# Performance work log

Measured on AMD Instinct MI355X. Metric: run time of the kernel, lower is better.

The kernel has to match this reference:

```python
import jax, jax.numpy as jnp
import numpy as np

NUM_HEADS = 16


def setup_inputs() -> dict:
    key = jax.random.key(0)
    ks = jax.random.split(key, 6)
    B, S, E = 2, 2048, 1024
    scale = 1.0 / np.sqrt(E)
    return {
        "x": jax.random.normal(ks[0], (B, S, E), dtype=jnp.float32),
        "mask": jnp.ones((B, S), dtype=jnp.int32),
        "Wq": jax.random.normal(ks[1], (E, E), dtype=jnp.float32) * scale,
        "bq": jnp.zeros((E,), dtype=jnp.float32),
        "Wk": jax.random.normal(ks[2], (E, E), dtype=jnp.float32) * scale,
        "bk": jnp.zeros((E,), dtype=jnp.float32),
        "Wv": jax.random.normal(ks[3], (E, E), dtype=jnp.float32) * scale,
        "bv": jnp.zeros((E,), dtype=jnp.float32),
        "Wo": jax.random.normal(ks[4], (E, E), dtype=jnp.float32) * scale,
        "bo": jnp.zeros((E,), dtype=jnp.float32),
    }


def reference(x, mask, Wq, bq, Wk, bk, Wv, bv, Wo, bo):
    B, S, E = x.shape
    H = NUM_HEADS
    D = E // H

    def heads(t):  # [B,S,E] -> [B,H,S,D]
        return t.reshape(B, S, H, D).transpose(0, 2, 1, 3)

    q = heads(x @ Wq + bq)
    k = heads(x @ Wk + bk)
    v = heads(x @ Wv + bv)

    # scaled dot-product scores [B,H,S,S]
    scores = jnp.einsum("bhsd,bhtd->bhst", q, k) / jnp.sqrt(jnp.float32(D))
    m = mask.astype(jnp.float32)[:, None, None, :]  # key-side padding mask
    scores = scores + (-1e9) * (1.0 - m)
    weights = jax.nn.softmax(scores, axis=-1)
    attn = jnp.einsum("bhst,bhtd->bhsd", weights, v)

    concat = attn.transpose(0, 2, 1, 3).reshape(B, S, E)
    return concat @ Wo + bo
```

## Files before the change

kernel.cpp:

```cpp
#include <hip/hip_runtime.h>
#include <stdint.h>

#define E_DIM   1024
#define HNUM    16
#define DH      64
#define BATCH   2
#define SEQ     2048
#define M_TOT   (BATCH*SEQ)
#define LOG2E   1.44269504088896340736f

typedef __bf16 bf16x8 __attribute__((ext_vector_type(8)));
typedef __bf16 bf16x4 __attribute__((ext_vector_type(4)));
typedef float  f32x4  __attribute__((ext_vector_type(4)));
typedef float  f32x16 __attribute__((ext_vector_type(16)));
typedef unsigned short u16;
typedef unsigned int   u32;
typedef unsigned long long u64;
typedef u16 u16x8 __attribute__((ext_vector_type(8)));
typedef u32 u32x2 __attribute__((ext_vector_type(2)));
typedef u32 u32x4 __attribute__((ext_vector_type(4)));

__device__ __forceinline__ u16 f2bf(float f) {
    u32 u = __builtin_bit_cast(u32, f);
    u32 r = 0x7FFFu + ((u >> 16) & 1u);
    return (u16)((u + r) >> 16);
}

__device__ __forceinline__ void gload_lds16(const u16* g, u16* l) {
    __builtin_amdgcn_global_load_lds(
        (const __attribute__((address_space(1))) u32*)g,
        (__attribute__((address_space(3))) u32*)l, 16, 0, 0);
}

__device__ __forceinline__ u32 cvt_pk_bf16(float lo, float hi) {
    u32 r;
    asm("v_cvt_pk_bf16_f32 %0, %1, %2" : "=v"(r) : "v"(lo), "v"(hi));
    return r;
}

#define MFMA16(a,b,c) __builtin_amdgcn_mfma_f32_16x16x32_bf16((a),(b),(c),0,0,0)
#define MFMA32(a,b,c) __builtin_amdgcn_mfma_f32_32x32x16_bf16((a),(b),(c),0,0,0)

__global__ __launch_bounds__(256) void cast_x_kernel(const float* __restrict__ x,
                                                     u16* __restrict__ out, int n) {
    int idx = (blockIdx.x * 256 + threadIdx.x) * 4;
    if (idx < n) {
        float4 v = *reinterpret_cast<const float4*>(x + idx);
        ushort4 o;
        o.x = f2bf(v.x); o.y = f2bf(v.y); o.z = f2bf(v.z); o.w = f2bf(v.w);
        *reinterpret_cast<ushort4*>(out + idx) = o;
    }
}

__global__ __launch_bounds__(256) void maskbits_kernel(const int* __restrict__ mask,
                                                       u64* __restrict__ bits) {
    int i = blockIdx.x * 256 + threadIdx.x;
    u64 bl = __ballot(mask[i] != 0);
    if ((i & 63) == 0) bits[i >> 6] = bl;
}

__global__ void wtrans_kernel(const float* __restrict__ w0, const float* __restrict__ w1,
                              const float* __restrict__ w2, const float* __restrict__ w3,
                              u16* __restrict__ out) {
    __shared__ float tile[32][33];
    const float* w = blockIdx.z == 0 ? w0 : blockIdx.z == 1 ? w1 : blockIdx.z == 2 ? w2 : w3;
    const int n0 = blockIdx.x * 32, k0 = blockIdx.y * 32;
    #pragma unroll
    for (int j = 0; j < 4; j++) {
        int k = k0 + threadIdx.y + j * 8;
        tile[threadIdx.y + j * 8][threadIdx.x] = w[(size_t)k * E_DIM + n0 + threadIdx.x];
    }
    __syncthreads();
    u16* o = out + (size_t)blockIdx.z * E_DIM * E_DIM;
    #pragma unroll
    for (int j = 0; j < 4; j++) {
        int n = n0 + threadIdx.y + j * 8;
        o[(size_t)n * E_DIM + k0 + threadIdx.x] = f2bf(tile[threadIdx.x][threadIdx.y + j * 8]);
    }
}

template <typename OutT>
__global__ __launch_bounds__(256) void gemm_kernel(
    const u16* __restrict__ A, const u16* __restrict__ Bt_base, OutT* __restrict__ C_base,
    const float* __restrict__ bias0, const float* __restrict__ bias1,
    const float* __restrict__ bias2, float scale0, int Mdim) {
    const int z = blockIdx.z;
    const u16* Bt = Bt_base + (size_t)z * E_DIM * E_DIM;
    OutT* C = C_base + (size_t)z * Mdim * E_DIM;
    const float* bias = (z == 0) ? bias0 : (z == 1 ? bias1 : bias2);
    const float scale = (z == 0) ? scale0 : 1.0f;

    __shared__ __align__(16) u16 Als[128 * 32];
    __shared__ __align__(16) u16 Bls[128 * 32];

    const int tid = threadIdx.x;
    const int lane = tid & 63;
    const int w = tid >> 6;
    const int wr = (w >> 1) * 64, wc = (w & 1) * 64;
    const int tm = blockIdx.y * 128, tn = blockIdx.x * 128;
    const int r4 = tid >> 2;
    const int c8 = (tid & 3) * 8;

    f32x4 acc[4][4] = {};

    for (int k0 = 0; k0 < E_DIM; k0 += 32) {
        gload_lds16(A + (size_t)(tm + r4) * E_DIM + k0 + c8, Als + tid * 8);
        gload_lds16(A + (size_t)(tm + 64 + r4) * E_DIM + k0 + c8, Als + 2048 + tid * 8);
        gload_lds16(Bt + (size_t)(tn + r4) * E_DIM + k0 + c8, Bls + tid * 8);
        gload_lds16(Bt + (size_t)(tn + 64 + r4) * E_DIM + k0 + c8, Bls + 2048 + tid * 8);
        __syncthreads();
        const int lr = lane & 15, lg = lane >> 4;
        bf16x8 af[4], bfr[4];
        #pragma unroll
        for (int m = 0; m < 4; m++)
            af[m] = *reinterpret_cast<const bf16x8*>(Als + (wr + m * 16 + lr) * 32 + lg * 8);
        #pragma unroll
        for (int n = 0; n < 4; n++)
            bfr[n] = *reinterpret_cast<const bf16x8*>(Bls + (wc + n * 16 + lr) * 32 + lg * 8);
        #pragma unroll
        for (int m = 0; m < 4; m++)
            #pragma unroll
            for (int n = 0; n < 4; n++)
                acc[m][n] = MFMA16(af[m], bfr[n], acc[m][n]);
        __syncthreads();
    }

    const int lr = lane & 15, lg = lane >> 4;
    #pragma unroll
    for (int m = 0; m < 4; m++) {
        #pragma unroll
        for (int n = 0; n < 4; n++) {
            const int col = tn + wc + n * 16 + lr;
            const float bv = bias[col];
            #pragma unroll
            for (int r = 0; r < 4; r++) {
                const int row = tm + wr + m * 16 + lg * 4 + r;
                float v = (acc[m][n][r] + bv) * scale;
                if constexpr (sizeof(OutT) == 2) {
                    C[(size_t)row * E_DIM + col] = f2bf(v);
                } else {
                    C[(size_t)row * E_DIM + col] = v;
                }
            }
        }
    }
}

__global__ __launch_bounds__(512) void attn_kernel(
    const u16* __restrict__ Q, const u16* __restrict__ K, const u16* __restrict__ V,
    const u64* __restrict__ mbits, u16* __restrict__ PO, float* __restrict__ lws) {
    __shared__ __align__(16) u16 Kls[4][64 * 64];
    __shared__ __align__(16) u16 Vt[2][64 * 64];

    const int tid = threadIdx.x;
    const int lane = tid & 63;
    const int wave = tid >> 6;
    const int sub = wave >> 2;
    const int wg = wave & 3;
    const int hi = lane >> 5;
    const int l31 = lane & 31;
    const int n = blockIdx.x;
    const int g = n & 63, qt = n >> 6;
    const int h = g & 15, zz = g >> 4;
    const int b = zz >> 1, half = zz & 1;

    const int qrow = b * SEQ + qt * 256 + sub * 128 + wg * 32 + l31;
    bf16x8 qf[4];
    #pragma unroll
    for (int kc = 0; kc < 4; kc++)
        qf[kc] = *reinterpret_cast<const bf16x8*>(Q + (size_t)qrow * E_DIM + h * DH + kc * 16 + hi * 8);

    const int krow = (l31 & 3) | ((l31 & 4) << 1) | ((l31 & 8) >> 1) | (l31 & 16);
    const u32 ksw = (u32)(krow & 7) << 4;
    u32 koff[4];
    #pragma unroll
    for (int kc = 0; kc < 4; kc++)
        koff[kc] = (((u32)krow * 128) + (u32)kc * 32 + (u32)hi * 16) ^ ksw;

    const int krA = tid >> 3;
    const int kcA = (tid & 7) ^ (krA & 7);
    const size_t kgoff = (size_t)krA * E_DIM + kcA * 8;

    const int t8 = tid & 255;
    const int vhalf = tid >> 8;
    const int vc = t8 & 7;
    const int vsg = ((t8 >> 3) ^ (vc << 2)) & 31;
    const size_t vgoff = (size_t)(2 * vsg) * E_DIM + vc * 8 + vhalf * 4;
    u32 vwoff[4];
    #pragma unroll
    for (int jj = 0; jj < 4; jj++) {
        const int j = vhalf * 4 + jj;
        vwoff[jj] = (((u32)(vc * 8 + j) * 128) + (u32)vsg * 4) ^ ((u32)j << 4);
    }
    u32 vroff[4];
    #pragma unroll
    for (int kc = 0; kc < 4; kc++)
        vroff[kc] = (((u32)l31 * 128) + (u32)(2 * kc + hi) * 16) ^ (((u32)(l31 & 7)) << 4);

    f32x16 oacc0 = {}, oacc1 = {};
    float l_run = 0.f;

    const u16* Kg = K + (size_t)(b * SEQ + half * (SEQ / 2)) * E_DIM + h * DH;
    const u16* Vg = V + (size_t)(b * SEQ + half * (SEQ / 2)) * E_DIM + h * DH;
    const size_t TSTEP = (size_t)64 * E_DIM;
    const u16* kgp = Kg + kgoff;
    const u16* vgp = Vg + vgoff;
    const int NT = SEQ / 2 / 64;

    {
        u32x2 a0 = *reinterpret_cast<const u32x2*>(vgp);
        u32x2 a1 = *reinterpret_cast<const u32x2*>(vgp + E_DIM);
        gload_lds16(kgp,             &Kls[0][tid * 8]);
        gload_lds16(kgp + TSTEP,     &Kls[1][tid * 8]);
        gload_lds16(kgp + 2 * TSTEP, &Kls[2][tid * 8]);
        kgp += 3 * TSTEP; vgp += TSTEP;
        asm volatile("s_waitcnt vmcnt(1)" ::: "memory");
        __builtin_amdgcn_sched_barrier(0);
        #pragma unroll
        for (int jj = 0; jj < 4; jj++)
            *(u32*)((char*)Vt + vwoff[jj]) = __builtin_amdgcn_perm(
                a1[jj >> 1], a0[jj >> 1], (jj & 1) ? 0x07060302u : 0x05040100u);
        asm volatile("s_waitcnt lgkmcnt(0)" ::: "memory");
        __builtin_amdgcn_sched_barrier(0);
        __builtin_amdgcn_s_barrier();
    }

    f32x16 sc0 = {}, sc1 = {};
    {
        const char* Kb = (const char*)Kls;
        __builtin_amdgcn_s_setprio(1);
        #pragma unroll
        for (int kc = 0; kc < 4; kc++) {
            bf16x8 kf0 = *(const bf16x8*)(Kb + koff[kc]);
            bf16x8 kf1 = *(const bf16x8*)(Kb + koff[kc] + 4096);
            sc0 = MFMA32(kf0, qf[kc], sc0);
            sc1 = MFMA32(kf1, qf[kc], sc1);
        }
        __builtin_amdgcn_s_setprio(0);
    }

    for (int t = 0; t < NT; t++) {
        const bool haveV = (t + 1 < NT);
        const bool haveK = (t + 3 < NT);
        u32x2 a0, a1;
        if (haveV) {
            a0 = *reinterpret_cast<const u32x2*>(vgp);
            a1 = *reinterpret_cast<const u32x2*>(vgp + E_DIM);
        }
        if (haveK) {
            gload_lds16(kgp, &Kls[(t + 3) & 3][tid * 8]);
        }

        const u64 mb = mbits[b * (SEQ / 64) + half * NT + t];
        if (mb != ~0ull) {
            #pragma unroll
            for (int r = 0; r < 16; r++) {
                const int key = (r & 3) + 4 * ((r >> 2) & 1) + 8 * hi + 16 * ((r >> 3) & 1);
                if (!((mb >> key) & 1))        sc0[r] += -1.442695e9f;
                if (!((mb >> (32 + key)) & 1)) sc1[r] += -1.442695e9f;
            }
        }
        float sum = 0.f;
        #pragma unroll
        for (int r = 0; r < 16; r++) {
            sc0[r] = __builtin_amdgcn_exp2f(sc0[r]); sum += sc0[r];
        }
        #pragma unroll
        for (int r = 0; r < 16; r++) {
            sc1[r] = __builtin_amdgcn_exp2f(sc1[r]); sum += sc1[r];
        }
        l_run += sum;

        bf16x8 pf[4];
        {
            u32x4 pw0, pw1, pw2, pw3;
            #pragma unroll
            for (int e = 0; e < 4; e++) {
                pw0[e] = cvt_pk_bf16(sc0[2 * e],     sc0[2 * e + 1]);
                pw1[e] = cvt_pk_bf16(sc0[8 + 2 * e], sc0[9 + 2 * e]);
                pw2[e] = cvt_pk_bf16(sc1[2 * e],     sc1[2 * e + 1]);
                pw3[e] = cvt_pk_bf16(sc1[8 + 2 * e], sc1[9 + 2 * e]);
            }
            pf[0] = __builtin_bit_cast(bf16x8, pw0);
            pf[1] = __builtin_bit_cast(bf16x8, pw1);
            pf[2] = __builtin_bit_cast(bf16x8, pw2);
            pf[3] = __builtin_bit_cast(bf16x8, pw3);
        }

        f32x16 sn0 = {}, sn1 = {};
        if (haveV) {
            const char* Kb = (const char*)Kls + ((t + 1) & 3) * 8192;
            __builtin_amdgcn_s_setprio(1);
            #pragma unroll
            for (int kc = 0; kc < 4; kc++) {
                bf16x8 kf0 = *(const bf16x8*)(Kb + koff[kc]);
                bf16x8 kf1 = *(const bf16x8*)(Kb + koff[kc] + 4096);
                sn0 = MFMA32(kf0, qf[kc], sn0);
                sn1 = MFMA32(kf1, qf[kc], sn1);
            }
            __builtin_amdgcn_s_setprio(0);
        }

        {
            const char* Vb = (const char*)Vt + (t & 1) * 8192;
            __builtin_amdgcn_s_setprio(1);
            #pragma unroll
            for (int kc = 0; kc < 4; kc++) {
                bf16x8 vf0 = *(const bf16x8*)(Vb + vroff[kc]);
                bf16x8 vf1 = *(const bf16x8*)(Vb + vroff[kc] + 4096);
                oacc0 = MFMA32(vf0, pf[kc], oacc0);
                oacc1 = MFMA32(vf1, pf[kc], oacc1);
            }
            __builtin_amdgcn_s_setprio(0);
        }

        asm volatile("s_waitcnt vmcnt(1)" ::: "memory");
        __builtin_amdgcn_sched_barrier(0);
        if (haveV) {
            #pragma unroll
            for (int jj = 0; jj < 4; jj++)
                *(u32*)((char*)Vt + ((t + 1) & 1) * 8192 + vwoff[jj]) = __builtin_amdgcn_perm(
                    a1[jj >> 1], a0[jj >> 1], (jj & 1) ? 0x07060302u : 0x05040100u);
        }
        asm volatile("s_waitcnt lgkmcnt(0)" ::: "memory");
        __builtin_amdgcn_sched_barrier(0);
        __builtin_amdgcn_s_barrier();

        sc0 = sn0; sc1 = sn1;
        if (haveK) { kgp += TSTEP; }
        if (haveV) { vgp += TSTEP; }
    }

    const float l_tot = l_run + __shfl_xor(l_run, 32);
    u16* op = PO + ((size_t)half * M_TOT + qrow) * E_DIM + h * DH;
    #pragma unroll
    for (int db = 0; db < 2; db++) {
        #pragma unroll
        for (int j = 0; j < 4; j++) {
            u32x2 pk;
            pk[0] = cvt_pk_bf16(db ? oacc1[4 * j + 0] : oacc0[4 * j + 0],
                                db ? oacc1[4 * j + 1] : oacc0[4 * j + 1]);
            pk[1] = cvt_pk_bf16(db ? oacc1[4 * j + 2] : oacc0[4 * j + 2],
                                db ? oacc1[4 * j + 3] : oacc0[4 * j + 3]);
            const int d0 = 32 * db + 8 * j + 4 * hi;
            *reinterpret_cast<u32x2*>(op + d0) = pk;
        }
    }
    if (hi == 0) lws[((size_t)half * M_TOT + qrow) * HNUM + h] = l_tot;
}

__global__ __launch_bounds__(256) void combine_kernel(const u16* __restrict__ PO,
                                                      const float* __restrict__ lws,
                                                      u16* __restrict__ ab) {
    const int i = (blockIdx.x * 256 + threadIdx.x) * 8;
    const int row = i >> 10;
    const int h = (i & 1023) >> 6;
    const float l0 = lws[(size_t)row * HNUM + h];
    const float l1 = lws[((size_t)M_TOT + row) * HNUM + h];
    const float rl = 1.0f / (l0 + l1);
    const bf16x8 a = *reinterpret_cast<const bf16x8*>(PO + i);
    const bf16x8 c = *reinterpret_cast<const bf16x8*>(PO + (size_t)M_TOT * E_DIM + i);
    u16x8 o;
    #pragma unroll
    for (int j = 0; j < 8; j++)
        o[j] = f2bf(((float)a[j] + (float)c[j]) * rl);
    *reinterpret_cast<u16x8*>(ab + i) = o;
}

extern "C" void kernel_launch(void* const* d_in, const int* in_sizes, int n_in,
                              void* d_out, int out_size, void* d_ws, size_t ws_size,
                              hipStream_t stream) {
    const float* x  = (const float*)d_in[0];
    const int* mask = (const int*)d_in[1];
    const float* Wq = (const float*)d_in[2];
    const float* bq = (const float*)d_in[3];
    const float* Wk = (const float*)d_in[4];
    const float* bk = (const float*)d_in[5];
    const float* Wv = (const float*)d_in[6];
    const float* bv = (const float*)d_in[7];
    const float* Wo = (const float*)d_in[8];
    const float* bo = (const float*)d_in[9];
    float* out = (float*)d_out;

    u16* ws  = (u16*)d_ws;
    const size_t ME = (size_t)M_TOT * E_DIM;
    u16* xb  = ws;
    u16* wt  = ws + ME;
    u16* qb  = ws + 2 * ME;
    u16* kbf = ws + 3 * ME;
    u16* vbf = ws + 4 * ME;
    u64* mbf = (u64*)(ws + 5 * ME);
    float* lws = (float*)(ws + 5 * ME + 8192);
    u16* ab  = xb;
    u16* po  = (u16*)d_out;

    cast_x_kernel<<<dim3(M_TOT * E_DIM / 1024), dim3(256), 0, stream>>>(x, xb, M_TOT * E_DIM);
    wtrans_kernel<<<dim3(E_DIM / 32, E_DIM / 32, 4), dim3(32, 8), 0, stream>>>(Wq, Wk, Wv, Wo, wt);
    maskbits_kernel<<<dim3(M_TOT / 256), dim3(256), 0, stream>>>(mask, mbf);
    gemm_kernel<u16><<<dim3(E_DIM / 128, M_TOT / 128, 3), dim3(256), 0, stream>>>(
        xb, wt, qb, bq, bk, bv, 0.125f * LOG2E, M_TOT);
    attn_kernel<<<dim3(512), dim3(512), 0, stream>>>(qb, kbf, vbf, mbf, po, lws);
    combine_kernel<<<dim3(M_TOT * E_DIM / 2048), dim3(256), 0, stream>>>(po, lws, ab);
    gemm_kernel<float><<<dim3(E_DIM / 128, M_TOT / 128, 1), dim3(256), 0, stream>>>(
        ab, wt + (size_t)3 * E_DIM * E_DIM, out, bo, bo, bo, 1.0f, M_TOT);
}
```

Before: 128.8 us.

## Add 256x128-tile triple-buffered GEMM for fused QKV projection

Replaces the QKV projection GEMM with a new kernel that uses 256x128 tiles, 512 threads, 32x32 MFMA instructions and a three-stage LDS pipeline fed by direct global-to-LDS loads with XOR-swizzled addressing. The epilogue packs bf16 outputs into 16-byte vector stores and picks the bias per Q/K/V slice. This aims to raise data reuse per tile and hide load latency behind compute. In exchange it uses more shared memory per block and launches fewer blocks, which may lower occupancy.

```diff
diff --git a/kernel.cpp b/kernel.cpp
--- a/kernel.cpp
+++ b/kernel.cpp
@@ -142,6 +142,119 @@
                     C[(size_t)row * E_DIM + col] = v;
                 }
             }
+        }
+    }
+}
+
+__global__ __launch_bounds__(512, 4) void gemm256_kernel(
+    const u16* __restrict__ A, const u16* __restrict__ Bt, u16* __restrict__ Cb,
+    const float* __restrict__ bias0, const float* __restrict__ bias1,
+    const float* __restrict__ bias2, float scale0) {
+    __shared__ __align__(16) u16 Als[3][256 * 32];
+    __shared__ __align__(16) u16 Bls[3][128 * 32];
+
+    const int tid = threadIdx.x;
+    const int lane = tid & 63;
+    const int w = tid >> 6;
+    const int hi = lane >> 5;
+    const int l31 = lane & 31;
+    const int tm = blockIdx.x * 256;
+    const int tn = blockIdx.y * 128;
+
+    const int krow = (l31 & 3) | ((l31 & 4) << 1) | ((l31 & 8) >> 1) | (l31 & 16);
+
+    u32 aoff[2];
+    #pragma unroll
+    for (int ks = 0; ks < 2; ks++) {
+        const u32 a = (u32)(w * 32 + l31) * 64 + ks * 32 + hi * 16;
+        aoff[ks] = a ^ (((a >> 7) & 7) << 4);
+    }
+    u32 boff[4][2];
+    #pragma unroll
+    for (int nt = 0; nt < 4; nt++)
+        #pragma unroll
+        for (int ks = 0; ks < 2; ks++) {
+            const u32 a = (u32)(nt * 32 + krow) * 64 + ks * 32 + hi * 16;
+            boff[nt][ks] = a ^ (((a >> 7) & 7) << 4);
+        }
+
+    size_t goffA0, goffA1, goffB;
+    {
+        u32 b0 = (u32)tid * 16;
+        u32 r0 = b0 ^ (((b0 >> 7) & 7) << 4);
+        goffA0 = (size_t)(r0 >> 6) * E_DIM + ((r0 & 63) >> 1);
+        u32 b1 = (u32)(tid + 512) * 16;
+        u32 r1 = b1 ^ (((b1 >> 7) & 7) << 4);
+        goffA1 = (size_t)(r1 >> 6) * E_DIM + ((r1 & 63) >> 1);
+        goffB = (size_t)(r0 >> 6) * E_DIM + ((r0 & 63) >> 1);
+    }
+
+    const u16* Ag = A + (size_t)tm * E_DIM;
+    const u16* Bg = Bt + (size_t)tn * E_DIM;
+
+    f32x16 acc[4] = {};
+
+    gload_lds16(Ag + goffA0, &Als[0][tid * 8]);
+    gload_lds16(Ag + goffA1, &Als[0][(tid + 512) * 8]);
+    gload_lds16(Bg + goffB, &Bls[0][tid * 8]);
+    gload_lds16(Ag + goffA0 + 32, &Als[1][tid * 8]);
+    gload_lds16(Ag + goffA1 + 32, &Als[1][(tid + 512) * 8]);
+    gload_lds16(Bg + goffB + 32, &Bls[1][tid * 8]);
+    asm volatile("s_waitcnt vmcnt(3)" ::: "memory");
+    __builtin_amdgcn_sched_barrier(0);
+    __builtin_amdgcn_s_barrier();
+
+    for (int k = 0; k < 32; k++) {
+        const int sl = k - (k / 3) * 3;
+        const int sp = (k + 2) - ((k + 2) / 3) * 3;
+        const size_t ko = (size_t)(k + 2) * 32;
+        gload_lds16(Ag + goffA0 + ko, &Als[sp][tid * 8]);
+        gload_lds16(Ag + goffA1 + ko, &Als[sp][(tid + 512) * 8]);
+        gload_lds16(Bg + goffB + ko, &Bls[sp][tid * 8]);
+
+        const char* Ab = (const char*)Als[sl];
+        const char* Bb = (const char*)Bls[sl];
+        __builtin_amdgcn_s_setprio(1);
+        #pragma unroll
+        for (int ks = 0; ks < 2; ks++) {
+            const bf16x8 af = *(const bf16x8*)(Ab + aoff[ks]);
+            #pragma unroll
+            for (int nt = 0; nt < 4; nt++) {
+                const bf16x8 bt = *(const bf16x8*)(Bb + boff[nt][ks]);
+                acc[nt] = MFMA32(bt, af, acc[nt]);
+            }
+        }
+        __builtin_amdgcn_s_setprio(0);
+
+        asm volatile("s_waitcnt vmcnt(3)" ::: "memory");
+        __builtin_amdgcn_sched_barrier(0);
+        __builtin_amdgcn_s_barrier();
+    }
+
+    const int slice = tn >> 10;
+    const float* bias = (slice == 0) ? bias0 : (slice == 1 ? bias1 : bias2);
+    const float scale = (slice == 0) ? scale0 : 1.0f;
+    const int m = tm + w * 32 + l31;
+    const int cb = tn & 1023;
+    u16* C = Cb + (size_t)slice * ((size_t)M_TOT * E_DIM) + (size_t)m * E_DIM + cb;
+    #pragma unroll
+    for (int nt = 0; nt < 4; nt++) {
+        #pragma unroll
+        for (int oct = 0; oct < 2; oct++) {
+            const int nb = nt * 32 + oct * 16 + hi * 8;
+            const f32x4 bv0 = *reinterpret_cast<const f32x4*>(bias + cb + nb);
+            const f32x4 bv1 = *reinterpret_cast<const f32x4*>(bias + cb + nb + 4);
+            const int r0 = oct * 8;
+            u32x4 pk;
+            pk[0] = cvt_pk_bf16((acc[nt][r0 + 0] + bv0[0]) * scale,
+                                (acc[nt][r0 + 1] + bv0[1]) * scale);
+            pk[1] = cvt_pk_bf16((acc[nt][r0 + 2] + bv0[2]) * scale,
+                                (acc[nt][r0 + 3] + bv0[3]) * scale);
+            pk[2] = cvt_pk_bf16((acc[nt][r0 + 4] + bv1[0]) * scale,
+                                (acc[nt][r0 + 5] + bv1[1]) * scale);
+            pk[3] = cvt_pk_bf16((acc[nt][r0 + 6] + bv1[2]) * scale,
+                                (acc[nt][r0 + 7] + bv1[3]) * scale);
+            *reinterpret_cast<u32x4*>(C + nb) = pk;
         }
     }
 }
@@ -397,8 +510,8 @@
     cast_x_kernel<<<dim3(M_TOT * E_DIM / 1024), dim3(256), 0, stream>>>(x, xb, M_TOT * E_DIM);
     wtrans_kernel<<<dim3(E_DIM / 32, E_DIM / 32, 4), dim3(32, 8), 0, stream>>>(Wq, Wk, Wv, Wo, wt);
     maskbits_kernel<<<dim3(M_TOT / 256), dim3(256), 0, stream>>>(mask, mbf);
-    gemm_kernel<u16><<<dim3(E_DIM / 128, M_TOT / 128, 3), dim3(256), 0, stream>>>(
-        xb, wt, qb, bq, bk, bv, 0.125f * LOG2E, M_TOT);
+    gemm256_kernel<<<dim3(M_TOT / 256, 3 * E_DIM / 128), dim3(512), 0, stream>>>(
+        xb, wt, qb, bq, bk, bv, 0.125f * LOG2E);
     attn_kernel<<<dim3(512), dim3(512), 0, stream>>>(qb, kbf, vbf, mbf, po, lws);
     combine_kernel<<<dim3(M_TOT * E_DIM / 2048), dim3(256), 0, stream>>>(po, lws, ab);
     gemm_kernel<float><<<dim3(E_DIM / 128, M_TOT / 128, 1), dim3(256), 0, stream>>>(
```

After: 136.3 us. 1.06x slower.
